# Optimization experiments

Measured on AMD Instinct MI355X. Metric: run time of the kernel, lower is better.

## Reference

```python
import jax, jax.numpy as jnp
import numpy as np

G = 512      # graphs per batch
PER = 800    # nodes per graph
N = G * PER  # total nodes
X = 256      # x_size (= h_size so layers compose)
H = 256      # h_size
VOCAB = 32000
NCLS = 104


def setup_inputs() -> dict:
    rng = np.random.default_rng(0)
    # Random tree per graph: node 0 is root, parent(i) uniform in [0, i)
    i_idx = np.arange(1, PER)
    parents = np.floor(rng.random((G, PER - 1)) * i_idx).astype(np.int64)
    base = (np.arange(G) * PER)[:, None]
    edge_dst = (parents + base).reshape(-1)                     # parent (message receiver)
    edge_src = (np.tile(np.arange(1, PER), (G, 1)) + base).reshape(-1)  # child
    E = edge_src.size
    child_count = np.bincount(edge_dst, minlength=N)
    # sort edges by (dst, src) so child position = rank among siblings
    order = np.lexsort((edge_src, edge_dst))
    edge_src = edge_src[order]
    edge_dst = edge_dst[order]
    starts = np.cumsum(child_count) - child_count
    pos = np.arange(E) - starts[edge_dst]
    n = child_count[edge_dst]
    # position-dependent interpolation coefficient: n==1 -> (W_l+W_r)/2 i.e. alpha=0.5
    alpha = np.where(n == 1, 0.5, pos / np.maximum(n - 1, 1)).astype(np.float32)

    node_type = rng.integers(0, VOCAB, N).astype(np.int32)
    graph_ids = np.repeat(np.arange(G), PER).astype(np.int32)

    key = jax.random.key(0)
    ks = jax.random.split(key, 6)
    s = 0.05
    emb = jax.random.normal(ks[0], (VOCAB, X), jnp.float32) * s
    W_left = jax.random.normal(ks[1], (X, H), jnp.float32) * s
    W_right = jax.random.normal(ks[2], (X, H), jnp.float32) * s
    W_top = jax.random.normal(ks[3], (X, H), jnp.float32) * s
    b_conv = jnp.zeros((H,), jnp.float32)
    gate_w = jax.random.normal(ks[4], (H, 1), jnp.float32) * s
    gate_b = jnp.zeros((1,), jnp.float32)
    cls_w = jax.random.normal(ks[5], (H, NCLS), jnp.float32) * s
    cls_b = jnp.zeros((NCLS,), jnp.float32)

    return dict(
        node_type=jnp.asarray(node_type), edge_src=jnp.asarray(edge_src.astype(np.int32)),
        edge_dst=jnp.asarray(edge_dst.astype(np.int32)), alpha=jnp.asarray(alpha),
        child_count=jnp.asarray(child_count.astype(np.int32)), graph_ids=jnp.asarray(graph_ids),
        emb=emb, W_left=W_left, W_right=W_right, W_top=W_top, b_conv=b_conv,
        gate_w=gate_w, gate_b=gate_b, cls_w=cls_w, cls_b=cls_b,
    )


def reference(node_type, edge_src, edge_dst, alpha, child_count, graph_ids,
              emb, W_left, W_right, W_top, b_conv,
              gate_w, gate_b, cls_w, cls_b):
    h = emb[node_type]                                  # [N, X]
    # TBCNN conv layer: sum_i ((1-a_i) W_left + a_i W_right) h_child_i
    #                 = (sum (1-a_i) h_i) W_left + (sum a_i h_i) W_right
    h_src = h[edge_src]                                 # [E, X]
    left = jax.ops.segment_sum(h_src * (1.0 - alpha)[:, None], edge_dst, num_segments=N)
    right = jax.ops.segment_sum(h_src * alpha[:, None], edge_dst, num_segments=N)
    conv = jax.nn.relu(left @ W_left + right @ W_right + h @ W_top + b_conv)
    # nodes without children receive no message -> keep embedding (DGL semantics)
    h = jnp.where((child_count > 0)[:, None], conv, h)  # [N, H]

    # GlobalAttentionPooling: per-graph softmax over gate scores
    gate = h @ gate_w + gate_b                          # [N, 1]
    gmax = jax.ops.segment_max(gate, graph_ids, num_segments=G)
    e = jnp.exp(gate - gmax[graph_ids])
    denom = jax.ops.segment_sum(e, graph_ids, num_segments=G)
    attn = e / denom[graph_ids]                         # [N, 1]
    pooled = jax.ops.segment_sum(h * attn, graph_ids, num_segments=G)  # [G, H]

    return pooled @ cls_w + cls_b                       # [G, NCLS]
```

## Files before the change

kernel.cpp:

```cpp
#include <hip/hip_runtime.h>
#include <stdint.h>

#define XH   256
#define NCLS 104
#define YW   768

typedef __attribute__((ext_vector_type(8))) short          short8;
typedef __attribute__((ext_vector_type(4))) float          floatx4;
typedef __attribute__((ext_vector_type(4))) unsigned short ushort4b;

__device__ __forceinline__ float bf2f(unsigned short u) {
    unsigned v = ((unsigned)u) << 16;
    return __builtin_bit_cast(float, v);
}
__device__ __forceinline__ unsigned short f2bf(float f) {
    unsigned v = __builtin_bit_cast(unsigned, f);
    unsigned r = (v + 0x7fffu + ((v >> 16) & 1u)) >> 16;
    return (unsigned short)r;
}
__device__ __forceinline__ void gll16(const void* g, void* l) {
    __builtin_amdgcn_global_load_lds(
        (const __attribute__((address_space(1))) unsigned*)g,
        (__attribute__((address_space(3))) unsigned*)l, 16, 0, 0);
}

__global__ __launch_bounds__(256)
void k_zero(int* __restrict__ p, int n) {
    int i = blockIdx.x * 256 + threadIdx.x;
    if (i < n) p[i] = 0;
}

__global__ __launch_bounds__(256)
void k_prep_all(const float* __restrict__ emb, const float* __restrict__ Wl,
                const float* __restrict__ Wr, const float* __restrict__ Wt,
                const int* __restrict__ edge_src, const int* __restrict__ edge_dst,
                const float* __restrict__ alpha, const int* __restrict__ node_type,
                unsigned short* __restrict__ embh, unsigned short* __restrict__ Btw,
                int2* __restrict__ epk, int* __restrict__ row_start,
                int vocab, int E) {
    int idx = blockIdx.x * 256 + threadIdx.x;
    int nA = vocab * (XH / 4);
    if (idx < nA) {
        floatx4 f = *(const floatx4*)&emb[(size_t)idx * 4];
        ushort4b u;
        #pragma unroll
        for (int i = 0; i < 4; i++) u[i] = f2bf(f[i]);
        *(ushort4b*)&embh[(size_t)idx * 4] = u;
        return;
    }
    idx -= nA;
    int nB = 3 * XH * XH;
    if (idx < nB) {
        int m = idx >> 16, r = idx & 65535, c = r >> 8, k = r & 255;
        const float* W = (m == 0) ? Wl : (m == 1) ? Wr : Wt;
        Btw[idx] = f2bf(W[k * XH + c]);
        return;
    }
    idx -= nB;
    if (idx < E) {
        int s = edge_src[idx];
        int2 p;
        p.x = node_type[s] * YW;
        p.y = __float_as_int(alpha[idx]);
        epk[idx] = p;
        int d = edge_dst[idx];
        if (idx == 0 || edge_dst[idx - 1] != d) row_start[d] = idx;
    }
}

__global__ __launch_bounds__(256)
void k_gemm(const unsigned short* __restrict__ embh,
            const unsigned short* __restrict__ Btw,
            unsigned short* __restrict__ Y) {
    const int m0 = blockIdx.x * 128;
    const int n0 = blockIdx.y * 128;
    const int tid  = threadIdx.x;
    const int lane = tid & 63;
    const int wv   = tid >> 6;
    const int mw   = wv >> 1;
    const int nw   = wv & 1;
    const int quad = lane >> 4;
    const int l15  = lane & 15;

    __shared__ __align__(16) unsigned short Ab[128 * 32];
    __shared__ __align__(16) unsigned short Bb[128 * 32];

    floatx4 acc[4][4];
    #pragma unroll
    for (int i = 0; i < 4; i++)
        #pragma unroll
        for (int j = 0; j < 4; j++) acc[i][j] = floatx4{0.f, 0.f, 0.f, 0.f};

    const int lq = lane >> 2;
    const int lb = (lane & 3) * 16;

    for (int kc = 0; kc < 8; kc++) {
        #pragma unroll
        for (int i = 0; i < 2; i++) {
            int issue = wv * 2 + i;
            int row   = issue * 16 + lq;
            gll16((const char*)embh + (size_t)(m0 + row) * 512 + kc * 64 + lb,
                  (char*)Ab + issue * 1024);
            gll16((const char*)Btw + (size_t)(n0 + row) * 512 + kc * 64 + lb,
                  (char*)Bb + issue * 1024);
        }
        __syncthreads();
        short8 a[4];
        #pragma unroll
        for (int mt = 0; mt < 4; mt++)
            a[mt] = *(const short8*)((const char*)Ab + (mw * 64 + mt * 16 + l15) * 64 + quad * 16);
        #pragma unroll
        for (int nt = 0; nt < 4; nt++) {
            short8 b = *(const short8*)((const char*)Bb + (nw * 64 + nt * 16 + l15) * 64 + quad * 16);
            #pragma unroll
            for (int mt = 0; mt < 4; mt++)
                acc[mt][nt] = __builtin_amdgcn_mfma_f32_16x16x32_bf16(a[mt], b, acc[mt][nt], 0, 0, 0);
        }
        __syncthreads();
    }

    #pragma unroll
    for (int nt = 0; nt < 4; nt++) {
        int col = n0 + nw * 64 + nt * 16 + l15;
        #pragma unroll
        for (int mt = 0; mt < 4; mt++) {
            #pragma unroll
            for (int r = 0; r < 4; r++) {
                int row = m0 + mw * 64 + mt * 16 + quad * 4 + r;
                Y[(size_t)row * YW + col] = f2bf(acc[mt][nt][r]);
            }
        }
    }
}

__global__ __launch_bounds__(512, 8)
void k_graph(const int* __restrict__ node_type, const int* __restrict__ child_count,
             const unsigned short* __restrict__ embh, const unsigned short* __restrict__ Y,
             const int2* __restrict__ epk, const int* __restrict__ row_start,
             const float* __restrict__ b_conv, const float* __restrict__ gate_w,
             const float* __restrict__ gate_b, float* __restrict__ pool_ws, int PER) {
    const int g    = blockIdx.x >> 1;
    const int half = blockIdx.x & 1;
    const int tid  = threadIdx.x;
    const int lane = tid & 63;
    const int wv   = tid >> 6;
    const int slot = half * 8 + wv;
    const int base = g * PER;

    __shared__ float pw[8 * XH];
    __shared__ float ds[8];

    float gw4[4], bc4[4];
    #pragma unroll
    for (int i = 0; i < 4; i++) gw4[i] = gate_w[4 * lane + i];
    #pragma unroll
    for (int i = 0; i < 4; i++) bc4[i] = b_conv[4 * lane + i];
    const float gb = gate_b[0];

    float acc4[4] = {0.f, 0.f, 0.f, 0.f};
    float dsum = 0.f;

    int vg = base + slot;
    int c  = child_count[vg];
    int tv = node_type[vg];
    int rs = row_start[vg];

    for (int v = slot; v < PER; v += 16) {
        int cn = 0, tvn = 0, rsn = 0;
        if (v + 16 < PER) {
            cn  = child_count[vg + 16];
            tvn = node_type[vg + 16];
            rsn = row_start[vg + 16];
        }

        float h4[4];
        if (c == 0) {
            ushort4b hv = *(const ushort4b*)&embh[(size_t)tv * XH + 4 * lane];
            #pragma unroll
            for (int i = 0; i < 4; i++) h4[i] = bf2f(hv[i]);
        } else {
            ushort4b yt = *(const ushort4b*)&Y[(size_t)tv * YW + 2 * XH + 4 * lane];
            float s4[4] = {0.f, 0.f, 0.f, 0.f};
            int e = rs, e1 = rs + c;
            for (; e + 2 <= e1; e += 2) {
                int2 p0 = epk[e], p1 = epk[e + 1];
                float a0 = __int_as_float(p0.y), a1 = __int_as_float(p1.y);
                int oL0 = p0.x + (a0 == 1.f ? XH : 0);
                int oR0 = p0.x + (a0 == 0.f ? 0 : XH);
                int oL1 = p1.x + (a1 == 1.f ? XH : 0);
                int oR1 = p1.x + (a1 == 0.f ? 0 : XH);
                ushort4b yl0 = *(const ushort4b*)&Y[(size_t)oL0 + 4 * lane];
                ushort4b yr0 = *(const ushort4b*)&Y[(size_t)oR0 + 4 * lane];
                ushort4b yl1 = *(const ushort4b*)&Y[(size_t)oL1 + 4 * lane];
                ushort4b yr1 = *(const ushort4b*)&Y[(size_t)oR1 + 4 * lane];
                float w0 = 1.f - a0, w1 = 1.f - a1;
                #pragma unroll
                for (int i = 0; i < 4; i++)
                    s4[i] += w0 * bf2f(yl0[i]) + a0 * bf2f(yr0[i])
                           + w1 * bf2f(yl1[i]) + a1 * bf2f(yr1[i]);
            }
            if (e < e1) {
                int2 p0 = epk[e];
                float a0 = __int_as_float(p0.y);
                int oL0 = p0.x + (a0 == 1.f ? XH : 0);
                int oR0 = p0.x + (a0 == 0.f ? 0 : XH);
                ushort4b yl0 = *(const ushort4b*)&Y[(size_t)oL0 + 4 * lane];
                ushort4b yr0 = *(const ushort4b*)&Y[(size_t)oR0 + 4 * lane];
                float w0 = 1.f - a0;
                #pragma unroll
                for (int i = 0; i < 4; i++)
                    s4[i] += w0 * bf2f(yl0[i]) + a0 * bf2f(yr0[i]);
            }
            #pragma unroll
            for (int i = 0; i < 4; i++)
                h4[i] = fmaxf(s4[i] + bf2f(yt[i]) + bc4[i], 0.f);
        }

        float sg = h4[0] * gw4[0] + h4[1] * gw4[1] + h4[2] * gw4[2] + h4[3] * gw4[3];
        #pragma unroll
        for (int o = 1; o < 64; o <<= 1) sg += __shfl_xor(sg, o);
        float ew = __expf(sg + gb);
        dsum += ew;
        #pragma unroll
        for (int i = 0; i < 4; i++) acc4[i] += ew * h4[i];

        c = cn; tv = tvn; rs = rsn; vg += 16;
    }

    #pragma unroll
    for (int i = 0; i < 4; i++) pw[wv * XH + 4 * lane + i] = acc4[i];
    if (lane == 0) ds[wv] = dsum;
    __syncthreads();

    if (tid < XH) {
        float p = 0.f;
        #pragma unroll
        for (int w = 0; w < 8; w++) p += pw[w * XH + tid];
        atomicAdd(&pool_ws[g * (XH + 1) + tid], p);
    } else if (tid == XH) {
        float d = 0.f;
        #pragma unroll
        for (int w = 0; w < 8; w++) d += ds[w];
        atomicAdd(&pool_ws[g * (XH + 1) + XH], d);
    }
}

__global__ __launch_bounds__(256)
void k_final(const float* __restrict__ pool_ws, const float* __restrict__ cls_w,
             const float* __restrict__ cls_b, float* __restrict__ out) {
    const int g = blockIdx.x, tid = threadIdx.x;
    __shared__ float pooled[XH];
    float d = pool_ws[g * (XH + 1) + XH];
    pooled[tid] = pool_ws[g * (XH + 1) + tid] / d;
    __syncthreads();
    if (tid < NCLS) {
        float o = cls_b[tid];
        #pragma unroll 8
        for (int k = 0; k < XH; k++) o += pooled[k] * cls_w[k * NCLS + tid];
        out[g * NCLS + tid] = o;
    }
}

extern "C" void kernel_launch(void* const* d_in, const int* in_sizes, int n_in,
                              void* d_out, int out_size, void* d_ws, size_t ws_size,
                              hipStream_t stream) {
    const int*   node_type   = (const int*)d_in[0];
    const int*   edge_src    = (const int*)d_in[1];
    const int*   edge_dst    = (const int*)d_in[2];
    const float* alpha       = (const float*)d_in[3];
    const int*   child_count = (const int*)d_in[4];
    const float* emb         = (const float*)d_in[6];
    const float* Wl          = (const float*)d_in[7];
    const float* Wr          = (const float*)d_in[8];
    const float* Wt          = (const float*)d_in[9];
    const float* b_conv      = (const float*)d_in[10];
    const float* gate_w      = (const float*)d_in[11];
    const float* gate_b      = (const float*)d_in[12];
    const float* cls_w       = (const float*)d_in[13];
    const float* cls_b       = (const float*)d_in[14];

    const int N     = in_sizes[0];
    const int E     = in_sizes[1];
    const int vocab = in_sizes[6] / XH;
    const int G     = out_size / NCLS;
    const int PER   = N / G;

    unsigned short* Y      = (unsigned short*)d_ws;
    unsigned short* embh   = Y + (size_t)vocab * YW;
    unsigned short* Btw    = embh + (size_t)vocab * XH;
    int2*           epk    = (int2*)(Btw + 3 * XH * XH);
    int*            row_start = (int*)(epk + E);
    float*          pool_ws   = (float*)(row_start + N);

    const int nzero = N + G * (XH + 1);
    hipLaunchKernelGGL(k_zero, dim3((nzero + 255) / 256), dim3(256), 0, stream,
                       row_start, nzero);

    const int nprep = vocab * (XH / 4) + 3 * XH * XH + E;
    hipLaunchKernelGGL(k_prep_all, dim3((nprep + 255) / 256), dim3(256), 0, stream,
                       emb, Wl, Wr, Wt, edge_src, edge_dst, alpha, node_type,
                       embh, Btw, epk, row_start, vocab, E);

    hipLaunchKernelGGL(k_gemm, dim3(vocab / 128, YW / 128), dim3(256), 0, stream,
                       embh, Btw, Y);

    hipLaunchKernelGGL(k_graph, dim3(2 * G), dim3(512), 0, stream,
                       node_type, child_count, embh, Y, epk, row_start,
                       b_conv, gate_w, gate_b, pool_ws, PER);

    hipLaunchKernelGGL(k_final, dim3(G), dim3(256), 0, stream,
                       pool_ws, cls_w, cls_b, (float*)d_out);
}
```

Measured before the change: 255.1 us.

## Interleave left/right projections, fold bias into GEMM, fuse pooling and classifier

The GEMM output is split into an interleaved left/right table and a separate top table, so each child edge needs one 16-byte gather instead of two 8-byte gathers. The conv bias is added in the GEMM epilogue. Each graph now runs in a single 1024-thread block that does the pooling normalisation and classifier itself, which removes the zero kernel, the atomics and the final kernel. Removing the zero kernel means row_start is no longer cleared, so it is only correct if every node with children gets its entry written. The larger blocks may also lower occupancy.

```diff
diff --git a/kernel.cpp b/kernel.cpp
--- a/kernel.cpp
+++ b/kernel.cpp
@@ -3,11 +3,11 @@
 
 #define XH   256
 #define NCLS 104
-#define YW   768
 
 typedef __attribute__((ext_vector_type(8))) short          short8;
 typedef __attribute__((ext_vector_type(4))) float          floatx4;
 typedef __attribute__((ext_vector_type(4))) unsigned short ushort4b;
+typedef __attribute__((ext_vector_type(8))) unsigned short ushort8b;
 
 __device__ __forceinline__ float bf2f(unsigned short u) {
     unsigned v = ((unsigned)u) << 16;
@@ -25,19 +25,13 @@
 }
 
 __global__ __launch_bounds__(256)
-void k_zero(int* __restrict__ p, int n) {
-    int i = blockIdx.x * 256 + threadIdx.x;
-    if (i < n) p[i] = 0;
-}
-
-__global__ __launch_bounds__(256)
-void k_prep_all(const float* __restrict__ emb, const float* __restrict__ Wl,
-                const float* __restrict__ Wr, const float* __restrict__ Wt,
-                const int* __restrict__ edge_src, const int* __restrict__ edge_dst,
-                const float* __restrict__ alpha, const int* __restrict__ node_type,
-                unsigned short* __restrict__ embh, unsigned short* __restrict__ Btw,
-                int2* __restrict__ epk, int* __restrict__ row_start,
-                int vocab, int E) {
+void k_prep(const float* __restrict__ emb, const float* __restrict__ Wl,
+            const float* __restrict__ Wr, const float* __restrict__ Wt,
+            const int* __restrict__ edge_src, const int* __restrict__ edge_dst,
+            const float* __restrict__ alpha, const int* __restrict__ node_type,
+            unsigned short* __restrict__ embh, unsigned short* __restrict__ Btw,
+            int2* __restrict__ epk, int* __restrict__ row_start,
+            int vocab, int E) {
     int idx = blockIdx.x * 256 + threadIdx.x;
     int nA = vocab * (XH / 4);
     if (idx < nA) {
@@ -51,7 +45,10 @@
     idx -= nA;
     int nB = 3 * XH * XH;
     if (idx < nB) {
-        int m = idx >> 16, r = idx & 65535, c = r >> 8, k = r & 255;
+        int n = idx >> 8, k = idx & 255;
+        int m, c;
+        if (n < 512) { m = n & 1; c = n >> 1; }
+        else         { m = 2;     c = n - 512; }
         const float* W = (m == 0) ? Wl : (m == 1) ? Wr : Wt;
         Btw[idx] = f2bf(W[k * XH + c]);
         return;
@@ -60,7 +57,7 @@
     if (idx < E) {
         int s = edge_src[idx];
         int2 p;
-        p.x = node_type[s] * YW;
+        p.x = node_type[s] * 512;
         p.y = __float_as_int(alpha[idx]);
         epk[idx] = p;
         int d = edge_dst[idx];
@@ -71,7 +68,8 @@
 __global__ __launch_bounds__(256)
 void k_gemm(const unsigned short* __restrict__ embh,
             const unsigned short* __restrict__ Btw,
-            unsigned short* __restrict__ Y) {
+            const float* __restrict__ b_conv,
+            unsigned short* __restrict__ Ylr, unsigned short* __restrict__ Yt) {
     const int m0 = blockIdx.x * 128;
     const int n0 = blockIdx.y * 128;
     const int tid  = threadIdx.x;
@@ -119,53 +117,56 @@
         __syncthreads();
     }
 
+    const bool isT = (n0 >= 512);
     #pragma unroll
     for (int nt = 0; nt < 4; nt++) {
         int col = n0 + nw * 64 + nt * 16 + l15;
+        float bias = isT ? b_conv[col - 512] : 0.f;
         #pragma unroll
         for (int mt = 0; mt < 4; mt++) {
             #pragma unroll
             for (int r = 0; r < 4; r++) {
                 int row = m0 + mw * 64 + mt * 16 + quad * 4 + r;
-                Y[(size_t)row * YW + col] = f2bf(acc[mt][nt][r]);
+                unsigned short val = f2bf(acc[mt][nt][r] + bias);
+                if (isT) Yt[(size_t)row * XH + (col - 512)] = val;
+                else     Ylr[(size_t)row * 512 + col] = val;
             }
         }
     }
 }
 
-__global__ __launch_bounds__(512, 8)
+__global__ __launch_bounds__(1024, 8)
 void k_graph(const int* __restrict__ node_type, const int* __restrict__ child_count,
-             const unsigned short* __restrict__ embh, const unsigned short* __restrict__ Y,
+             const unsigned short* __restrict__ embh,
+             const unsigned short* __restrict__ Ylr, const unsigned short* __restrict__ Yt,
              const int2* __restrict__ epk, const int* __restrict__ row_start,
-             const float* __restrict__ b_conv, const float* __restrict__ gate_w,
-             const float* __restrict__ gate_b, float* __restrict__ pool_ws, int PER) {
-    const int g    = blockIdx.x >> 1;
-    const int half = blockIdx.x & 1;
+             const float* __restrict__ gate_w, const float* __restrict__ gate_b,
+             const float* __restrict__ cls_w, const float* __restrict__ cls_b,
+             float* __restrict__ out, int PER) {
+    const int g    = blockIdx.x;
     const int tid  = threadIdx.x;
     const int lane = tid & 63;
     const int wv   = tid >> 6;
-    const int slot = half * 8 + wv;
     const int base = g * PER;
 
-    __shared__ float pw[8 * XH];
-    __shared__ float ds[8];
-
-    float gw4[4], bc4[4];
+    __shared__ float pw[16 * XH];
+    __shared__ float ds[16];
+    __shared__ float pooled[XH];
+
+    float gw4[4];
     #pragma unroll
     for (int i = 0; i < 4; i++) gw4[i] = gate_w[4 * lane + i];
-    #pragma unroll
-    for (int i = 0; i < 4; i++) bc4[i] = b_conv[4 * lane + i];
     const float gb = gate_b[0];
 
     float acc4[4] = {0.f, 0.f, 0.f, 0.f};
     float dsum = 0.f;
 
-    int vg = base + slot;
+    int vg = base + wv;
     int c  = child_count[vg];
     int tv = node_type[vg];
     int rs = row_start[vg];
 
-    for (int v = slot; v < PER; v += 16) {
+    for (int v = wv; v < PER; v += 16) {
         int cn = 0, tvn = 0, rsn = 0;
         if (v + 16 < PER) {
             cn  = child_count[vg + 16];
@@ -179,41 +180,38 @@
             #pragma unroll
             for (int i = 0; i < 4; i++) h4[i] = bf2f(hv[i]);
         } else {
-            ushort4b yt = *(const ushort4b*)&Y[(size_t)tv * YW + 2 * XH + 4 * lane];
+            ushort4b yt = *(const ushort4b*)&Yt[(size_t)tv * XH + 4 * lane];
             float s4[4] = {0.f, 0.f, 0.f, 0.f};
             int e = rs, e1 = rs + c;
             for (; e + 2 <= e1; e += 2) {
                 int2 p0 = epk[e], p1 = epk[e + 1];
+                ushort8b w0 = *(const ushort8b*)&Ylr[(size_t)p0.x + 8 * lane];
+                ushort8b w1 = *(const ushort8b*)&Ylr[(size_t)p1.x + 8 * lane];
                 float a0 = __int_as_float(p0.y), a1 = __int_as_float(p1.y);
-                int oL0 = p0.x + (a0 == 1.f ? XH : 0);
-                int oR0 = p0.x + (a0 == 0.f ? 0 : XH);
-                int oL1 = p1.x + (a1 == 1.f ? XH : 0);
-                int oR1 = p1.x + (a1 == 0.f ? 0 : XH);
-                ushort4b yl0 = *(const ushort4b*)&Y[(size_t)oL0 + 4 * lane];
-                ushort4b yr0 = *(const ushort4b*)&Y[(size_t)oR0 + 4 * lane];
-                ushort4b yl1 = *(const ushort4b*)&Y[(size_t)oL1 + 4 * lane];
-                ushort4b yr1 = *(const ushort4b*)&Y[(size_t)oR1 + 4 * lane];
-                float w0 = 1.f - a0, w1 = 1.f - a1;
                 #pragma unroll
-                for (int i = 0; i < 4; i++)
-                    s4[i] += w0 * bf2f(yl0[i]) + a0 * bf2f(yr0[i])
-                           + w1 * bf2f(yl1[i]) + a1 * bf2f(yr1[i]);
+                for (int i = 0; i < 4; i++) {
+                    float l0 = bf2f(w0[2 * i]), r0 = bf2f(w0[2 * i + 1]);
+                    s4[i] += l0 + a0 * (r0 - l0);
+                }
+                #pragma unroll
+                for (int i = 0; i < 4; i++) {
+                    float l1 = bf2f(w1[2 * i]), r1 = bf2f(w1[2 * i + 1]);
+                    s4[i] += l1 + a1 * (r1 - l1);
+                }
             }
             if (e < e1) {
                 int2 p0 = epk[e];
+                ushort8b w0 = *(const ushort8b*)&Ylr[(size_t)p0.x + 8 * lane];
                 float a0 = __int_as_float(p0.y);
-                int oL0 = p0.x + (a0 == 1.f ? XH : 0);
-                int oR0 = p0.x + (a0 == 0.f ? 0 : XH);
-                ushort4b yl0 = *(const ushort4b*)&Y[(size_t)oL0 + 4 * lane];
-                ushort4b yr0 = *(const ushort4b*)&Y[(size_t)oR0 + 4 * lane];
-                float w0 = 1.f - a0;
                 #pragma unroll
-                for (int i = 0; i < 4; i++)
-                    s4[i] += w0 * bf2f(yl0[i]) + a0 * bf2f(yr0[i]);
+                for (int i = 0; i < 4; i++) {
+                    float l0 = bf2f(w0[2 * i]), r0 = bf2f(w0[2 * i + 1]);
+                    s4[i] += l0 + a0 * (r0 - l0);
+                }
             }
             #pragma unroll
             for (int i = 0; i < 4; i++)
-                h4[i] = fmaxf(s4[i] + bf2f(yt[i]) + bc4[i], 0.f);
+                h4[i] = fmaxf(s4[i] + bf2f(yt[i]), 0.f);
         }
 
         float sg = h4[0] * gw4[0] + h4[1] * gw4[1] + h4[2] * gw4[2] + h4[3] * gw4[3];
@@ -233,26 +231,15 @@
     __syncthreads();
 
     if (tid < XH) {
-        float p = 0.f;
-        #pragma unroll
-        for (int w = 0; w < 8; w++) p += pw[w * XH + tid];
-        atomicAdd(&pool_ws[g * (XH + 1) + tid], p);
-    } else if (tid == XH) {
-        float d = 0.f;
-        #pragma unroll
-        for (int w = 0; w < 8; w++) d += ds[w];
-        atomicAdd(&pool_ws[g * (XH + 1) + XH], d);
-    }
-}
-
-__global__ __launch_bounds__(256)
-void k_final(const float* __restrict__ pool_ws, const float* __restrict__ cls_w,
-             const float* __restrict__ cls_b, float* __restrict__ out) {
-    const int g = blockIdx.x, tid = threadIdx.x;
-    __shared__ float pooled[XH];
-    float d = pool_ws[g * (XH + 1) + XH];
-    pooled[tid] = pool_ws[g * (XH + 1) + tid] / d;
+        float p = 0.f, d = 0.f;
+        #pragma unroll
+        for (int w = 0; w < 16; w++) p += pw[w * XH + tid];
+        #pragma unroll
+        for (int w = 0; w < 16; w++) d += ds[w];
+        pooled[tid] = p / d;
+    }
     __syncthreads();
+
     if (tid < NCLS) {
         float o = cls_b[tid];
         #pragma unroll 8
@@ -285,29 +272,22 @@
     const int G     = out_size / NCLS;
     const int PER   = N / G;
 
-    unsigned short* Y      = (unsigned short*)d_ws;
-    unsigned short* embh   = Y + (size_t)vocab * YW;
-    unsigned short* Btw    = embh + (size_t)vocab * XH;
-    int2*           epk    = (int2*)(Btw + 3 * XH * XH);
+    unsigned short* Ylr  = (unsigned short*)d_ws;
+    unsigned short* Yt   = Ylr + (size_t)vocab * 512;
+    unsigned short* embh = Yt + (size_t)vocab * XH;
+    unsigned short* Btw  = embh + (size_t)vocab * XH;
+    int2*           epk  = (int2*)(Btw + 3 * XH * XH);
     int*            row_start = (int*)(epk + E);
-    float*          pool_ws   = (float*)(row_start + N);
-
-    const int nzero = N + G * (XH + 1);
-    hipLaunchKernelGGL(k_zero, dim3((nzero + 255) / 256), dim3(256), 0, stream,
-                       row_start, nzero);
 
     const int nprep = vocab * (XH / 4) + 3 * XH * XH + E;
-    hipLaunchKernelGGL(k_prep_all, dim3((nprep + 255) / 256), dim3(256), 0, stream,
+    hipLaunchKernelGGL(k_prep, dim3((nprep + 255) / 256), dim3(256), 0, stream,
                        emb, Wl, Wr, Wt, edge_src, edge_dst, alpha, node_type,
                        embh, Btw, epk, row_start, vocab, E);
 
-    hipLaunchKernelGGL(k_gemm, dim3(vocab / 128, YW / 128), dim3(256), 0, stream,
-                       embh, Btw, Y);
-
-    hipLaunchKernelGGL(k_graph, dim3(2 * G), dim3(512), 0, stream,
-                       node_type, child_count, embh, Y, epk, row_start,
-                       b_conv, gate_w, gate_b, pool_ws, PER);
-
-    hipLaunchKernelGGL(k_final, dim3(G), dim3(256), 0, stream,
-                       pool_ws, cls_w, cls_b, (float*)d_out);
-}
+    hipLaunchKernelGGL(k_gemm, dim3(vocab / 128, 6), dim3(256), 0, stream,
+                       embh, Btw, b_conv, Ylr, Yt);
+
+    hipLaunchKernelGGL(k_graph, dim3(G), dim3(1024), 0, stream,
+                       node_type, child_count, embh, Ylr, Yt, epk, row_start,
+                       gate_w, gate_b, cls_w, cls_b, (float*)d_out, PER);
+}
```

After: 243.5 us. -4.5%, faster.
